# Kernel tuning notes

Measured on AMD Instinct MI355X. Metric: run time of the kernel, lower is better.

## Reference

```python
import jax, jax.numpy as jnp
import numpy as np

EPS = 1e-3  # Keras BatchNormalization default epsilon


def _bn(x, gamma, beta, mean, var):
    # inference-mode batchnorm over channel axis 1 of [N,C,T,V]
    s = (gamma * jax.lax.rsqrt(var + EPS)).reshape(1, -1, 1, 1)
    b = (beta - gamma * mean * jax.lax.rsqrt(var + EPS)).reshape(1, -1, 1, 1)
    return x * s + b


def setup_inputs() -> dict:
    key = jax.random.key(0)
    ks = jax.random.split(key, 10)
    N, C, T, V, K, F, KT = 64, 64, 300, 25, 3, 64, 9
    x = jax.random.normal(ks[0], (N, C, T, V), jnp.float32)
    W1 = jax.random.normal(ks[1], (C, F * K), jnp.float32) * 0.05
    b1 = jnp.zeros((F * K,), jnp.float32)
    A = jax.random.normal(ks[2], (K, T, V, V), jnp.float32) * 0.2
    gamma1 = jnp.ones((F,), jnp.float32)
    beta1 = jnp.zeros((F,), jnp.float32)
    mean1 = jax.random.normal(ks[3], (F,), jnp.float32) * 0.1
    var1 = jax.random.uniform(ks[4], (F,), jnp.float32) + 0.5
    Wt = jax.random.normal(ks[5], (KT, 1, F, F), jnp.float32) * 0.05  # HWIO
    bt = jnp.zeros((F,), jnp.float32)
    gamma2 = jnp.ones((F,), jnp.float32)
    beta2 = jnp.zeros((F,), jnp.float32)
    mean2 = jax.random.normal(ks[6], (F,), jnp.float32) * 0.1
    var2 = jax.random.uniform(ks[7], (F,), jnp.float32) + 0.5
    return dict(x=x, W1=W1, b1=b1, A=A, gamma1=gamma1, beta1=beta1,
                mean1=mean1, var1=var1, Wt=Wt, bt=bt, gamma2=gamma2,
                beta2=beta2, mean2=mean2, var2=var2)


def reference(x, W1, b1, A, gamma1, beta1, mean1, var1, Wt, bt,
              gamma2, beta2, mean2, var2):
    N, C, T, V = x.shape
    K = A.shape[0]
    F = W1.shape[1] // K
    # SGTACN: 1x1 conv (channels_first) == channel matmul
    y = jnp.einsum('nctv,cf->nftv', x, W1) + b1.reshape(1, -1, 1, 1)
    y = y.reshape(N, K, F, T, V)
    # spatial graph contraction with learned per-timestep adjacency
    y = jnp.einsum('nkftv,ktvw->nftw', y, A)
    # tgcn: BN -> relu -> temporal conv [9,1] SAME -> BN
    y = jax.nn.relu(_bn(y, gamma1, beta1, mean1, var1))
    y = jax.lax.conv_general_dilated(
        y, Wt, window_strides=(1, 1), padding='SAME',
        dimension_numbers=('NCHW', 'HWIO', 'NCHW')) + bt.reshape(1, -1, 1, 1)
    y = _bn(y, gamma2, beta2, mean2, var2)
    # identity residual (stride=1, no downsample, C_in == filters) + relu
    return jax.nn.relu(y + x)
```

## Files before the change

### kernel.cpp

```cpp
#include <hip/hip_runtime.h>
#include <hip/hip_bf16.h>
#include <stdint.h>

#define EPS 1e-3f

typedef __attribute__((ext_vector_type(8))) short bf16x8;
typedef __attribute__((ext_vector_type(4))) float f32x4;

__device__ inline uint32_t pk2(float a, float b) {
    __hip_bfloat162 p;
    p.x = __float2bfloat16(a);
    p.y = __float2bfloat16(b);
    return *(uint32_t*)&p;
}

__global__ __launch_bounds__(256) void k0_prep_small(
    const float* __restrict__ W1, const float* __restrict__ Wt,
    const float* __restrict__ A,
    uint16_t* __restrict__ W1t, uint16_t* __restrict__ Abf,
    float* __restrict__ csA_g)
{
    int i = blockIdx.x * 256 + threadIdx.x;
    if (i < 12288) {
        int f = i / 192, Kp = i % 192, k = Kp >> 6, c = Kp & 63;
        __hip_bfloat16 b = __float2bfloat16(W1[c * 192 + k * 64 + f]);
        W1t[i] = *(uint16_t*)&b;
    } else if (i < 49152) {
        int j = i - 12288;
        int jj = j & 7, fo = (j >> 3) & 63, kb = j >> 9;
        int kk = kb * 8 + jj, dt = kk >> 6, fi = kk & 63;
        __hip_bfloat16 b = __float2bfloat16(Wt[(dt * 64 + fi) * 64 + fo]);
        Abf[j] = *(uint16_t*)&b;
    } else if (i < 71652) {
        int j = i - 49152;
        int k = j / 7500, r = j % 7500;
        int t = r / 25, w = r % 25;
        float s = 0.f;
        for (int v = 0; v < 25; ++v)
            s += A[((k * 300 + t) * 25 + v) * 25 + w];
        csA_g[j] = s;
    }
}

__global__ __launch_bounds__(256) void k0_prep_At(
    const float* __restrict__ A, uint16_t* __restrict__ At_g)
{
    int i = blockIdx.x * 256 + threadIdx.x;
    if (i < 921600) {
        int v = i & 31, w = (i >> 5) & 31, rest = i >> 10;
        int t = rest % 300, k = rest / 300;
        float val = 0.f;
        if (v < 25 && w < 25)
            val = A[((k * 300 + t) * 25 + v) * 25 + w];
        __hip_bfloat16 b = __float2bfloat16(val);
        At_g[i] = *(uint16_t*)&b;
    }
}

#define K1_SMEM 39680
__global__ __launch_bounds__(256, 4) void k1_wave(
    const float* __restrict__ x, const uint16_t* __restrict__ At_g,
    const uint16_t* __restrict__ W1t, const float* __restrict__ csA_g,
    const float* __restrict__ b1,
    const float* __restrict__ gamma1, const float* __restrict__ beta1,
    const float* __restrict__ mean1, const float* __restrict__ var1,
    uint32_t* __restrict__ h2u)
{
    extern __shared__ __align__(16) char smem[];
    float* s1s   = (float*)(smem + 38400);
    float* b1ns  = (float*)(smem + 38656);
    float* b1s   = (float*)(smem + 38912);

    const int t0   = blockIdx.x * 4;
    const int n    = blockIdx.y;
    const int tid  = threadIdx.x;
    const int lane = tid & 63, wv = tid >> 6;
    const int l15  = lane & 15, g = lane >> 4;
    const int t    = t0 + wv;
    char* slab = smem + wv * 9600;

    bf16x8 bfr[6];
    #pragma unroll
    for (int nf = 0; nf < 6; ++nf) {
        const int col = nf * 16 + l15;
        const int k = col >> 5, w = col & 31;
        bfr[nf] = *(const bf16x8*)(At_g + (((k * 300 + t) * 32 + w) * 32 + g * 8));
    }

    const float* xb = x + (size_t)n * 480000 + t * 25;
    float xr8[4][8];
    float x24v[4];
    #pragma unroll
    for (int mf = 0; mf < 4; ++mf) {
        const int c = l15 + 16 * mf;
        const float* xr = xb + (size_t)c * 7500;
        if (g < 3) {
            const float* p = xr + g * 8;
            #pragma unroll
            for (int j = 0; j < 8; ++j) xr8[mf][j] = p[j];
        } else {
            x24v[mf] = xr[24];
        }
    }

    float cs[2][3];
    #pragma unroll
    for (int q = 0; q < 2; ++q) {
        const int w = q * 16 + l15;
        const int wc = (w < 25) ? w : 24;
        const int ci = t * 25 + wc;
        cs[q][0] = csA_g[ci];
        cs[q][1] = csA_g[7500 + ci];
        cs[q][2] = csA_g[15000 + ci];
    }

    __builtin_amdgcn_sched_barrier(0);

    if (tid < 64) {
        float rs = rsqrtf(var1[tid] + EPS);
        s1s[tid]  = gamma1[tid] * rs;
        b1ns[tid] = beta1[tid] - gamma1[tid] * mean1[tid] * rs;
    }
    if (tid >= 64 && tid < 256) b1s[tid - 64] = b1[tid - 64];
    __syncthreads();

    bf16x8 a[4];
    #pragma unroll
    for (int mf = 0; mf < 4; ++mf) {
        union { bf16x8 v; uint32_t u[4]; } ua;
        if (g < 3) {
            ua.u[0] = pk2(xr8[mf][0], xr8[mf][1]);
            ua.u[1] = pk2(xr8[mf][2], xr8[mf][3]);
            ua.u[2] = pk2(xr8[mf][4], xr8[mf][5]);
            ua.u[3] = pk2(xr8[mf][6], xr8[mf][7]);
        } else {
            ua.u[0] = pk2(x24v[mf], 0.f);
            ua.u[1] = 0; ua.u[2] = 0; ua.u[3] = 0;
        }
        a[mf] = ua.v;
    }

    #pragma unroll
    for (int hh = 0; hh < 2; ++hh) {
        f32x4 acc[4][3];
        #pragma unroll
        for (int mf = 0; mf < 4; ++mf)
            #pragma unroll
            for (int nf3 = 0; nf3 < 3; ++nf3)
                acc[mf][nf3] = (f32x4){0.f, 0.f, 0.f, 0.f};

        #pragma unroll
        for (int nf3 = 0; nf3 < 3; ++nf3) {
            const int nf = hh * 3 + nf3;
            acc[0][nf3] = __builtin_amdgcn_mfma_f32_16x16x32_bf16(a[0], bfr[nf], acc[0][nf3], 0, 0, 0);
            acc[1][nf3] = __builtin_amdgcn_mfma_f32_16x16x32_bf16(a[1], bfr[nf], acc[1][nf3], 0, 0, 0);
            acc[2][nf3] = __builtin_amdgcn_mfma_f32_16x16x32_bf16(a[2], bfr[nf], acc[2][nf3], 0, 0, 0);
            acc[3][nf3] = __builtin_amdgcn_mfma_f32_16x16x32_bf16(a[3], bfr[nf], acc[3][nf3], 0, 0, 0);
        }

        #pragma unroll
        for (int nf3 = 0; nf3 < 3; ++nf3) {
            const int col = (hh * 3 + nf3) * 16 + l15;
            const int k = col >> 5, w = col & 31;
            if (w < 25) {
                const int sw = (w & 7) << 4;
                #pragma unroll
                for (int mf = 0; mf < 4; ++mf) {
                    const int c0 = mf * 16 + g * 4;
                    const int off = w * 384 + (((k * 64 + c0) * 2) ^ sw);
                    uint2 val;
                    val.x = pk2(acc[mf][nf3][0], acc[mf][nf3][1]);
                    val.y = pk2(acc[mf][nf3][2], acc[mf][nf3][3]);
                    *(uint2*)(slab + off) = val;
                }
            }
        }
    }

    bf16x8 azc[4];
    #pragma unroll
    for (int mf = 0; mf < 4; ++mf)
        azc[mf] = *(const bf16x8*)(W1t + (l15 + 16 * mf) * 192 + g * 8);

    asm volatile("s_waitcnt lgkmcnt(0)" ::: "memory");
    __builtin_amdgcn_sched_barrier(0);

    int wq[2], qaddr[2], qswz[2];
    #pragma unroll
    for (int q = 0; q < 2; ++q) {
        int w = q * 16 + l15;
        wq[q] = w;
        int wc = (w < 25) ? w : 24;
        qaddr[q] = wc * 384;
        qswz[q]  = (wc & 7) << 4;
    }

    f32x4 accz[4][2];
    #pragma unroll
    for (int mf = 0; mf < 4; ++mf)
        #pragma unroll
        for (int q = 0; q < 2; ++q)
            accz[mf][q] = (f32x4){0.f, 0.f, 0.f, 0.f};

    #pragma unroll
    for (int kb = 0; kb < 6; ++kb) {
        bf16x8 azn[4];
        if (kb < 5) {
            #pragma unroll
            for (int mf = 0; mf < 4; ++mf)
                azn[mf] = *(const bf16x8*)(W1t + (l15 + 16 * mf) * 192 + (kb + 1) * 32 + g * 8);
        }
        #pragma unroll
        for (int q = 0; q < 2; ++q) {
            bf16x8 b = *(const bf16x8*)(slab + qaddr[q] + ((kb * 64 + g * 16) ^ qswz[q]));
            accz[0][q] = __builtin_amdgcn_mfma_f32_16x16x32_bf16(azc[0], b, accz[0][q], 0, 0, 0);
            accz[1][q] = __builtin_amdgcn_mfma_f32_16x16x32_bf16(azc[1], b, accz[1][q], 0, 0, 0);
            accz[2][q] = __builtin_amdgcn_mfma_f32_16x16x32_bf16(azc[2], b, accz[2][q], 0, 0, 0);
            accz[3][q] = __builtin_amdgcn_mfma_f32_16x16x32_bf16(azc[3], b, accz[3][q], 0, 0, 0);
        }
        if (kb < 5) {
            #pragma unroll
            for (int mf = 0; mf < 4; ++mf) azc[mf] = azn[mf];
        }
    }

    const uint32_t tb = (uint32_t)(n * 300 + t);
    #pragma unroll
    for (int q = 0; q < 2; ++q) {
        const int w = wq[q];
        if (w < 25) {
            const uint32_t rowbase = tb * 800 + w * 32;
            #pragma unroll
            for (int mf = 0; mf < 4; ++mf) {
                const int f0 = mf * 16 + g * 4;
                float zz[4];
                #pragma unroll
                for (int rg = 0; rg < 4; ++rg) {
                    const int f = f0 + rg;
                    float z = accz[mf][q][rg]
                            + b1s[f] * cs[q][0] + b1s[64 + f] * cs[q][1]
                            + b1s[128 + f] * cs[q][2];
                    z = z * s1s[f] + b1ns[f];
                    zz[rg] = fmaxf(z, 0.f);
                }
                uint2 st;
                st.x = pk2(zz[0], zz[1]);
                st.y = pk2(zz[2], zz[3]);
                *(uint2*)(h2u + rowbase + (f0 >> 1)) = st;
            }
        }
    }
}

#define K2_SMEM 51712
__global__ __launch_bounds__(256, 3) void k2_mfma(
    const char* __restrict__ h2b,
    const uint16_t* __restrict__ Abf,
    const float* __restrict__ bt,
    const float* __restrict__ gamma2, const float* __restrict__ beta2,
    const float* __restrict__ mean2,  const float* __restrict__ var2,
    const float* __restrict__ x,
    float* __restrict__ out)
{
    extern __shared__ __align__(16) char smem2[];
    char*  lds_h = smem2;
    float* s2s   = (float*)(smem2 + 51200);
    float* b2s   = s2s + 64;

    const int t0  = blockIdx.x * 8;
    const int n   = blockIdx.y;
    const int tid = threadIdx.x;

    const size_t hn = (size_t)n * 300 * 3200;
    int4 tmp[13];
    #pragma unroll
    for (int i = 0; i < 13; ++i) {
        const int c = tid + i * 256;
        tmp[i] = make_int4(0, 0, 0, 0);
        if (c < 3200) {
            int rr = c >> 3, c8 = c & 7;
            int trow = rr / 25;
            int w = rr - trow * 25;
            int tg = t0 - 4 + trow;
            if (tg >= 0 && tg < 300)
                tmp[i] = *(const int4*)(h2b + hn + (size_t)tg * 3200 + w * 128 + (c8 << 4));
        }
    }
    __builtin_amdgcn_sched_barrier(0);

    if (tid < 64) {
        float rs = rsqrtf(var2[tid] + EPS);
        float s  = gamma2[tid] * rs;
        s2s[tid] = s;
        b2s[tid] = beta2[tid] - gamma2[tid] * mean2[tid] * rs + bt[tid] * s;
    }

    #pragma unroll
    for (int i = 0; i < 13; ++i) {
        const int c = tid + i * 256;
        if (c < 3200) {
            int s = c << 4;
            *(int4*)(lds_h + (s ^ (((s >> 7) & 7) << 4))) = tmp[i];
        }
    }
    __syncthreads();

    const int wv = tid >> 6, lane = tid & 63;
    const int l15 = lane & 15, g = lane >> 4;
    const int nMf = (wv == 0) ? 4 : 3;

    int rbase[4];
    #pragma unroll
    for (int q = 0; q < 4; ++q) {
        int col = (q * 4 + wv) * 16 + l15;
        rbase[q] = (col < 200) ? col : 199;
    }

    f32x4 acc[4][4];
    #pragma unroll
    for (int q = 0; q < 4; ++q)
        #pragma unroll
        for (int mf = 0; mf < 4; ++mf)
            acc[q][mf] = (f32x4){0.f, 0.f, 0.f, 0.f};

    bf16x8 wc_[4];
    #pragma unroll
    for (int mf = 0; mf < 4; ++mf)
        wc_[mf] = *(const bf16x8*)(Abf + ((0 * 4 + g) * 64 + l15 + mf * 16) * 8);

    for (int kk = 0; kk < 18; ++kk) {
        const int dt   = kk >> 1;
        const int half = (kk & 1) << 6;
        bf16x8 wn_[4];
        if (kk < 17) {
            const int kbn = (kk + 1) * 4 + g;
            #pragma unroll
            for (int mf = 0; mf < 4; ++mf)
                wn_[mf] = *(const bf16x8*)(Abf + (kbn * 64 + l15 + mf * 16) * 8);
        }
        #pragma unroll
        for (int q = 0; q < 4; ++q) {
            if (q < nMf) {
                int r = rbase[q] + 25 * dt;
                int s = (r << 7) + half + (g << 4);
                bf16x8 hfr = *(const bf16x8*)(lds_h + (s ^ ((r & 7) << 4)));
                acc[q][0] = __builtin_amdgcn_mfma_f32_16x16x32_bf16(hfr, wc_[0], acc[q][0], 0, 0, 0);
                acc[q][1] = __builtin_amdgcn_mfma_f32_16x16x32_bf16(hfr, wc_[1], acc[q][1], 0, 0, 0);
                acc[q][2] = __builtin_amdgcn_mfma_f32_16x16x32_bf16(hfr, wc_[2], acc[q][2], 0, 0, 0);
                acc[q][3] = __builtin_amdgcn_mfma_f32_16x16x32_bf16(hfr, wc_[3], acc[q][3], 0, 0, 0);
            }
        }
        if (kk < 17) {
            #pragma unroll
            for (int mf = 0; mf < 4; ++mf) wc_[mf] = wn_[mf];
        }
    }

    const size_t outn = (size_t)n * 480000;
    const int base = t0 * 25;
    const int vcols = (7500 - base < 200) ? (7500 - base) : 200;

    float4 xrv[4][4];
    #pragma unroll
    for (int q = 0; q < 4; ++q) {
        const int col0 = (q * 4 + wv) * 16 + g * 4;
        if (q < nMf && col0 < vcols) {
            #pragma unroll
            for (int mf = 0; mf < 4; ++mf) {
                const int fo = mf * 16 + l15;
                xrv[q][mf] = *(const float4*)(x + outn + (size_t)fo * 7500 + base + col0);
            }
        }
    }
    __builtin_amdgcn_sched_barrier(0);

    #pragma unroll
    for (int q = 0; q < 4; ++q) {
        const int col0 = (q * 4 + wv) * 16 + g * 4;
        if (q < nMf && col0 < vcols) {
            #pragma unroll
            for (int mf = 0; mf < 4; ++mf) {
                const int fo = mf * 16 + l15;
                const size_t ga = outn + (size_t)fo * 7500 + base + col0;
                const float s2 = s2s[fo], b2 = b2s[fo];
                float4 o;
                o.x = fmaxf(acc[q][mf][0] * s2 + b2 + xrv[q][mf].x, 0.f);
                o.y = fmaxf(acc[q][mf][1] * s2 + b2 + xrv[q][mf].y, 0.f);
                o.z = fmaxf(acc[q][mf][2] * s2 + b2 + xrv[q][mf].z, 0.f);
                o.w = fmaxf(acc[q][mf][3] * s2 + b2 + xrv[q][mf].w, 0.f);
                *(float4*)(out + ga) = o;
            }
        }
    }
}

extern "C" void kernel_launch(void* const* d_in, const int* in_sizes, int n_in,
                              void* d_out, int out_size, void* d_ws, size_t ws_size,
                              hipStream_t stream) {
    const float* x      = (const float*)d_in[0];
    const float* W1     = (const float*)d_in[1];
    const float* b1     = (const float*)d_in[2];
    const float* A      = (const float*)d_in[3];
    const float* gamma1 = (const float*)d_in[4];
    const float* beta1  = (const float*)d_in[5];
    const float* mean1  = (const float*)d_in[6];
    const float* var1   = (const float*)d_in[7];
    const float* Wt     = (const float*)d_in[8];
    const float* bt     = (const float*)d_in[9];
    const float* gamma2 = (const float*)d_in[10];
    const float* beta2  = (const float*)d_in[11];
    const float* mean2  = (const float*)d_in[12];
    const float* var2   = (const float*)d_in[13];
    float* out = (float*)d_out;

    char* ws = (char*)d_ws;
    uint32_t* h2u   = (uint32_t*)ws;
    char*     h2b   = ws;
    uint16_t* At_g  = (uint16_t*)(ws + 61440000);
    uint16_t* W1t   = (uint16_t*)(ws + 63283200);
    uint16_t* Abf   = (uint16_t*)(ws + 63307776);
    float*    csA_g = (float*)   (ws + 63381504);

    hipFuncSetAttribute((const void*)k1_wave,
                        hipFuncAttributeMaxDynamicSharedMemorySize, K1_SMEM);
    hipFuncSetAttribute((const void*)k2_mfma,
                        hipFuncAttributeMaxDynamicSharedMemorySize, K2_SMEM);

    k0_prep_small<<<280, 256, 0, stream>>>(W1, Wt, A, W1t, Abf, csA_g);
    k0_prep_At<<<3600, 256, 0, stream>>>(A, At_g);
    k1_wave<<<dim3(75, 64), 256, K1_SMEM, stream>>>(
        x, At_g, W1t, csA_g, b1, gamma1, beta1, mean1, var1, h2u);
    k2_mfma<<<dim3(38, 64), 256, K2_SMEM, stream>>>(
        h2b, Abf, bt, gamma2, beta2, mean2, var2, x, out);
}
```

Measured before the change: 402.7 us.

## Process five timesteps per wave with prefetch, merge prep kernels

The first compute kernel now gives each wave five consecutive timesteps instead of one. The next timestep's adjacency and input values are loaded from global memory while the current timestep's second GEMM runs, and the block count drops accordingly. The two preprocessing kernels are merged into a single launch. The cost is fewer blocks (960), which lowers parallelism, plus more register pressure from the prefetch buffers.

Result: slower. 572.3 us (+42.1%).

```diff
diff --git a/kernel.cpp b/kernel.cpp
--- a/kernel.cpp
+++ b/kernel.cpp
@@ -14,46 +14,43 @@
     return *(uint32_t*)&p;
 }
 
-__global__ __launch_bounds__(256) void k0_prep_small(
+__global__ __launch_bounds__(256) void k0_prep(
     const float* __restrict__ W1, const float* __restrict__ Wt,
     const float* __restrict__ A,
     uint16_t* __restrict__ W1t, uint16_t* __restrict__ Abf,
-    float* __restrict__ csA_g)
+    float* __restrict__ csA_g, uint16_t* __restrict__ At_g)
 {
-    int i = blockIdx.x * 256 + threadIdx.x;
-    if (i < 12288) {
-        int f = i / 192, Kp = i % 192, k = Kp >> 6, c = Kp & 63;
-        __hip_bfloat16 b = __float2bfloat16(W1[c * 192 + k * 64 + f]);
-        W1t[i] = *(uint16_t*)&b;
-    } else if (i < 49152) {
-        int j = i - 12288;
-        int jj = j & 7, fo = (j >> 3) & 63, kb = j >> 9;
-        int kk = kb * 8 + jj, dt = kk >> 6, fi = kk & 63;
-        __hip_bfloat16 b = __float2bfloat16(Wt[(dt * 64 + fi) * 64 + fo]);
-        Abf[j] = *(uint16_t*)&b;
-    } else if (i < 71652) {
-        int j = i - 49152;
-        int k = j / 7500, r = j % 7500;
-        int t = r / 25, w = r % 25;
-        float s = 0.f;
-        for (int v = 0; v < 25; ++v)
-            s += A[((k * 300 + t) * 25 + v) * 25 + w];
-        csA_g[j] = s;
-    }
-}
-
-__global__ __launch_bounds__(256) void k0_prep_At(
-    const float* __restrict__ A, uint16_t* __restrict__ At_g)
-{
-    int i = blockIdx.x * 256 + threadIdx.x;
-    if (i < 921600) {
+    const int b = blockIdx.x;
+    if (b < 3600) {
+        int i = b * 256 + threadIdx.x;
         int v = i & 31, w = (i >> 5) & 31, rest = i >> 10;
         int t = rest % 300, k = rest / 300;
         float val = 0.f;
         if (v < 25 && w < 25)
             val = A[((k * 300 + t) * 25 + v) * 25 + w];
-        __hip_bfloat16 b = __float2bfloat16(val);
-        At_g[i] = *(uint16_t*)&b;
+        __hip_bfloat16 bb = __float2bfloat16(val);
+        At_g[i] = *(uint16_t*)&bb;
+    } else {
+        int i = (b - 3600) * 256 + threadIdx.x;
+        if (i < 12288) {
+            int f = i / 192, Kp = i % 192, k = Kp >> 6, c = Kp & 63;
+            __hip_bfloat16 bb = __float2bfloat16(W1[c * 192 + k * 64 + f]);
+            W1t[i] = *(uint16_t*)&bb;
+        } else if (i < 49152) {
+            int j = i - 12288;
+            int jj = j & 7, fo = (j >> 3) & 63, kb = j >> 9;
+            int kk = kb * 8 + jj, dt = kk >> 6, fi = kk & 63;
+            __hip_bfloat16 bb = __float2bfloat16(Wt[(dt * 64 + fi) * 64 + fo]);
+            Abf[j] = *(uint16_t*)&bb;
+        } else if (i < 71652) {
+            int j = i - 49152;
+            int k = j / 7500, r = j % 7500;
+            int t = r / 25, w = r % 25;
+            float s = 0.f;
+            for (int v = 0; v < 25; ++v)
+                s += A[((k * 300 + t) * 25 + v) * 25 + w];
+            csA_g[j] = s;
+        }
     }
 }
 
@@ -71,50 +68,13 @@
     float* b1ns  = (float*)(smem + 38656);
     float* b1s   = (float*)(smem + 38912);
 
-    const int t0   = blockIdx.x * 4;
+    const int t0   = blockIdx.x * 20;
     const int n    = blockIdx.y;
     const int tid  = threadIdx.x;
     const int lane = tid & 63, wv = tid >> 6;
     const int l15  = lane & 15, g = lane >> 4;
-    const int t    = t0 + wv;
+    const int tw0  = t0 + wv * 5;
     char* slab = smem + wv * 9600;
-
-    bf16x8 bfr[6];
-    #pragma unroll
-    for (int nf = 0; nf < 6; ++nf) {
-        const int col = nf * 16 + l15;
-        const int k = col >> 5, w = col & 31;
-        bfr[nf] = *(const bf16x8*)(At_g + (((k * 300 + t) * 32 + w) * 32 + g * 8));
-    }
-
-    const float* xb = x + (size_t)n * 480000 + t * 25;
-    float xr8[4][8];
-    float x24v[4];
-    #pragma unroll
-    for (int mf = 0; mf < 4; ++mf) {
-        const int c = l15 + 16 * mf;
-        const float* xr = xb + (size_t)c * 7500;
-        if (g < 3) {
-            const float* p = xr + g * 8;
-            #pragma unroll
-            for (int j = 0; j < 8; ++j) xr8[mf][j] = p[j];
-        } else {
-            x24v[mf] = xr[24];
-        }
-    }
-
-    float cs[2][3];
-    #pragma unroll
-    for (int q = 0; q < 2; ++q) {
-        const int w = q * 16 + l15;
-        const int wc = (w < 25) ? w : 24;
-        const int ci = t * 25 + wc;
-        cs[q][0] = csA_g[ci];
-        cs[q][1] = csA_g[7500 + ci];
-        cs[q][2] = csA_g[15000 + ci];
-    }
-
-    __builtin_amdgcn_sched_barrier(0);
 
     if (tid < 64) {
         float rs = rsqrtf(var1[tid] + EPS);
@@ -124,131 +84,159 @@
     if (tid >= 64 && tid < 256) b1s[tid - 64] = b1[tid - 64];
     __syncthreads();
 
-    bf16x8 a[4];
-    #pragma unroll
-    for (int mf = 0; mf < 4; ++mf) {
-        union { bf16x8 v; uint32_t u[4]; } ua;
-        if (g < 3) {
-            ua.u[0] = pk2(xr8[mf][0], xr8[mf][1]);
-            ua.u[1] = pk2(xr8[mf][2], xr8[mf][3]);
-            ua.u[2] = pk2(xr8[mf][4], xr8[mf][5]);
-            ua.u[3] = pk2(xr8[mf][6], xr8[mf][7]);
-        } else {
-            ua.u[0] = pk2(x24v[mf], 0.f);
-            ua.u[1] = 0; ua.u[2] = 0; ua.u[3] = 0;
-        }
-        a[mf] = ua.v;
-    }
-
-    #pragma unroll
-    for (int hh = 0; hh < 2; ++hh) {
-        f32x4 acc[4][3];
+    bf16x8 bfrN[6];
+    float  xr8[4][8];
+    float  x24v[4];
+    bf16x8 aN[4];
+
+    auto LOADT = [&](int t) {
+        #pragma unroll
+        for (int nf = 0; nf < 6; ++nf) {
+            const int col = nf * 16 + l15;
+            const int k = col >> 5, w = col & 31;
+            bfrN[nf] = *(const bf16x8*)(At_g + (((k * 300 + t) * 32 + w) * 32 + g * 8));
+        }
+        const float* xb = x + (size_t)n * 480000 + t * 25;
+        #pragma unroll
+        for (int mf = 0; mf < 4; ++mf) {
+            const int c = l15 + 16 * mf;
+            const float* xr = xb + (size_t)c * 7500;
+            if (g < 3) {
+                const float* p = xr + g * 8;
+                #pragma unroll
+                for (int j = 0; j < 8; ++j) xr8[mf][j] = p[j];
+            } else {
+                x24v[mf] = xr[24];
+            }
+        }
+    };
+    auto CONV = [&]() {
+        #pragma unroll
+        for (int mf = 0; mf < 4; ++mf) {
+            union { bf16x8 v; uint32_t u[4]; } ua;
+            if (g < 3) {
+                ua.u[0] = pk2(xr8[mf][0], xr8[mf][1]);
+                ua.u[1] = pk2(xr8[mf][2], xr8[mf][3]);
+                ua.u[2] = pk2(xr8[mf][4], xr8[mf][5]);
+                ua.u[3] = pk2(xr8[mf][6], xr8[mf][7]);
+            } else {
+                ua.u[0] = pk2(x24v[mf], 0.f);
+                ua.u[1] = 0; ua.u[2] = 0; ua.u[3] = 0;
+            }
+            aN[mf] = ua.v;
+        }
+    };
+
+    LOADT(tw0);
+    CONV();
+
+    #pragma unroll
+    for (int i = 0; i < 5; ++i) {
+        const int t = tw0 + i;
+
+        #pragma unroll
+        for (int hh = 0; hh < 2; ++hh) {
+            f32x4 acc[4][3];
+            #pragma unroll
+            for (int mf = 0; mf < 4; ++mf)
+                #pragma unroll
+                for (int nf3 = 0; nf3 < 3; ++nf3)
+                    acc[mf][nf3] = (f32x4){0.f, 0.f, 0.f, 0.f};
+
+            #pragma unroll
+            for (int nf3 = 0; nf3 < 3; ++nf3) {
+                const int nf = hh * 3 + nf3;
+                acc[0][nf3] = __builtin_amdgcn_mfma_f32_16x16x32_bf16(aN[0], bfrN[nf], acc[0][nf3], 0, 0, 0);
+                acc[1][nf3] = __builtin_amdgcn_mfma_f32_16x16x32_bf16(aN[1], bfrN[nf], acc[1][nf3], 0, 0, 0);
+                acc[2][nf3] = __builtin_amdgcn_mfma_f32_16x16x32_bf16(aN[2], bfrN[nf], acc[2][nf3], 0, 0, 0);
+                acc[3][nf3] = __builtin_amdgcn_mfma_f32_16x16x32_bf16(aN[3], bfrN[nf], acc[3][nf3], 0, 0, 0);
+            }
+
+            #pragma unroll
+            for (int nf3 = 0; nf3 < 3; ++nf3) {
+                const int col = (hh * 3 + nf3) * 16 + l15;
+                const int k = col >> 5, w = col & 31;
+                if (w < 25) {
+                    const int sw = (w & 7) << 4;
+                    #pragma unroll
+                    for (int mf = 0; mf < 4; ++mf) {
+                        const int c0 = mf * 16 + g * 4;
+                        const int off = w * 384 + (((k * 64 + c0) * 2) ^ sw);
+                        uint2 val;
+                        val.x = pk2(acc[mf][nf3][0], acc[mf][nf3][1]);
+                        val.y = pk2(acc[mf][nf3][2], acc[mf][nf3][3]);
+                        *(uint2*)(slab + off) = val;
+                    }
+                }
+            }
+        }
+
+        if (i < 4) LOADT(t + 1);
+
+        f32x4 accz[4][2];
         #pragma unroll
         for (int mf = 0; mf < 4; ++mf)
             #pragma unroll
-            for (int nf3 = 0; nf3 < 3; ++nf3)
-                acc[mf][nf3] = (f32x4){0.f, 0.f, 0.f, 0.f};
-
-        #pragma unroll
-        for (int nf3 = 0; nf3 < 3; ++nf3) {
-            const int nf = hh * 3 + nf3;
-            acc[0][nf3] = __builtin_amdgcn_mfma_f32_16x16x32_bf16(a[0], bfr[nf], acc[0][nf3], 0, 0, 0);
-            acc[1][nf3] = __builtin_amdgcn_mfma_f32_16x16x32_bf16(a[1], bfr[nf], acc[1][nf3], 0, 0, 0);
-            acc[2][nf3] = __builtin_amdgcn_mfma_f32_16x16x32_bf16(a[2], bfr[nf], acc[2][nf3], 0, 0, 0);
-            acc[3][nf3] = __builtin_amdgcn_mfma_f32_16x16x32_bf16(a[3], bfr[nf], acc[3][nf3], 0, 0, 0);
-        }
-
-        #pragma unroll
-        for (int nf3 = 0; nf3 < 3; ++nf3) {
-            const int col = (hh * 3 + nf3) * 16 + l15;
-            const int k = col >> 5, w = col & 31;
+            for (int q = 0; q < 2; ++q)
+                accz[mf][q] = (f32x4){0.f, 0.f, 0.f, 0.f};
+
+        int qaddr[2], qswz[2];
+        #pragma unroll
+        for (int q = 0; q < 2; ++q) {
+            int w = q * 16 + l15;
+            int wc = (w < 25) ? w : 24;
+            qaddr[q] = wc * 384;
+            qswz[q]  = (wc & 7) << 4;
+        }
+
+        #pragma unroll
+        for (int kb = 0; kb < 6; ++kb) {
+            bf16x8 az[4];
+            #pragma unroll
+            for (int mf = 0; mf < 4; ++mf)
+                az[mf] = *(const bf16x8*)(W1t + (l15 + 16 * mf) * 192 + kb * 32 + g * 8);
+            #pragma unroll
+            for (int q = 0; q < 2; ++q) {
+                bf16x8 b = *(const bf16x8*)(slab + qaddr[q] + ((kb * 64 + g * 16) ^ qswz[q]));
+                accz[0][q] = __builtin_amdgcn_mfma_f32_16x16x32_bf16(az[0], b, accz[0][q], 0, 0, 0);
+                accz[1][q] = __builtin_amdgcn_mfma_f32_16x16x32_bf16(az[1], b, accz[1][q], 0, 0, 0);
+                accz[2][q] = __builtin_amdgcn_mfma_f32_16x16x32_bf16(az[2], b, accz[2][q], 0, 0, 0);
+                accz[3][q] = __builtin_amdgcn_mfma_f32_16x16x32_bf16(az[3], b, accz[3][q], 0, 0, 0);
+            }
+        }
+
+        const uint32_t tb = (uint32_t)(n * 300 + t);
+        #pragma unroll
+        for (int q = 0; q < 2; ++q) {
+            const int w = q * 16 + l15;
             if (w < 25) {
-                const int sw = (w & 7) << 4;
+                const int ci = t * 25 + w;
+                const float cs0 = csA_g[ci];
+                const float cs1 = csA_g[7500 + ci];
+                const float cs2 = csA_g[15000 + ci];
+                const uint32_t rowbase = tb * 800 + w * 32;
                 #pragma unroll
                 for (int mf = 0; mf < 4; ++mf) {
-                    const int c0 = mf * 16 + g * 4;
-                    const int off = w * 384 + (((k * 64 + c0) * 2) ^ sw);
-                    uint2 val;
-                    val.x = pk2(acc[mf][nf3][0], acc[mf][nf3][1]);
-                    val.y = pk2(acc[mf][nf3][2], acc[mf][nf3][3]);
-                    *(uint2*)(slab + off) = val;
+                    const int f0 = mf * 16 + g * 4;
+                    float zz[4];
+                    #pragma unroll
+                    for (int rg = 0; rg < 4; ++rg) {
+                        const int f = f0 + rg;
+                        float z = accz[mf][q][rg]
+                                + b1s[f] * cs0 + b1s[64 + f] * cs1
+                                + b1s[128 + f] * cs2;
+                        z = z * s1s[f] + b1ns[f];
+                        zz[rg] = fmaxf(z, 0.f);
+                    }
+                    uint2 st;
+                    st.x = pk2(zz[0], zz[1]);
+                    st.y = pk2(zz[2], zz[3]);
+                    *(uint2*)(h2u + rowbase + (f0 >> 1)) = st;
                 }
             }
         }
-    }
-
-    bf16x8 azc[4];
-    #pragma unroll
-    for (int mf = 0; mf < 4; ++mf)
-        azc[mf] = *(const bf16x8*)(W1t + (l15 + 16 * mf) * 192 + g * 8);
-
-    asm volatile("s_waitcnt lgkmcnt(0)" ::: "memory");
-    __builtin_amdgcn_sched_barrier(0);
-
-    int wq[2], qaddr[2], qswz[2];
-    #pragma unroll
-    for (int q = 0; q < 2; ++q) {
-        int w = q * 16 + l15;
-        wq[q] = w;
-        int wc = (w < 25) ? w : 24;
-        qaddr[q] = wc * 384;
-        qswz[q]  = (wc & 7) << 4;
-    }
-
-    f32x4 accz[4][2];
-    #pragma unroll
-    for (int mf = 0; mf < 4; ++mf)
-        #pragma unroll
-        for (int q = 0; q < 2; ++q)
-            accz[mf][q] = (f32x4){0.f, 0.f, 0.f, 0.f};
-
-    #pragma unroll
-    for (int kb = 0; kb < 6; ++kb) {
-        bf16x8 azn[4];
-        if (kb < 5) {
-            #pragma unroll
-            for (int mf = 0; mf < 4; ++mf)
-                azn[mf] = *(const bf16x8*)(W1t + (l15 + 16 * mf) * 192 + (kb + 1) * 32 + g * 8);
-        }
-        #pragma unroll
-        for (int q = 0; q < 2; ++q) {
-            bf16x8 b = *(const bf16x8*)(slab + qaddr[q] + ((kb * 64 + g * 16) ^ qswz[q]));
-            accz[0][q] = __builtin_amdgcn_mfma_f32_16x16x32_bf16(azc[0], b, accz[0][q], 0, 0, 0);
-            accz[1][q] = __builtin_amdgcn_mfma_f32_16x16x32_bf16(azc[1], b, accz[1][q], 0, 0, 0);
-            accz[2][q] = __builtin_amdgcn_mfma_f32_16x16x32_bf16(azc[2], b, accz[2][q], 0, 0, 0);
-            accz[3][q] = __builtin_amdgcn_mfma_f32_16x16x32_bf16(azc[3], b, accz[3][q], 0, 0, 0);
-        }
-        if (kb < 5) {
-            #pragma unroll
-            for (int mf = 0; mf < 4; ++mf) azc[mf] = azn[mf];
-        }
-    }
-
-    const uint32_t tb = (uint32_t)(n * 300 + t);
-    #pragma unroll
-    for (int q = 0; q < 2; ++q) {
-        const int w = wq[q];
-        if (w < 25) {
-            const uint32_t rowbase = tb * 800 + w * 32;
-            #pragma unroll
-            for (int mf = 0; mf < 4; ++mf) {
-                const int f0 = mf * 16 + g * 4;
-                float zz[4];
-                #pragma unroll
-                for (int rg = 0; rg < 4; ++rg) {
-                    const int f = f0 + rg;
-                    float z = accz[mf][q][rg]
-                            + b1s[f] * cs[q][0] + b1s[64 + f] * cs[q][1]
-                            + b1s[128 + f] * cs[q][2];
-                    z = z * s1s[f] + b1ns[f];
-                    zz[rg] = fmaxf(z, 0.f);
-                }
-                uint2 st;
-                st.x = pk2(zz[0], zz[1]);
-                st.y = pk2(zz[2], zz[3]);
-                *(uint2*)(h2u + rowbase + (f0 >> 1)) = st;
-            }
-        }
+
+        if (i < 4) CONV();
     }
 }
 
@@ -426,9 +414,8 @@
     hipFuncSetAttribute((const void*)k2_mfma,
                         hipFuncAttributeMaxDynamicSharedMemorySize, K2_SMEM);
 
-    k0_prep_small<<<280, 256, 0, stream>>>(W1, Wt, A, W1t, Abf, csA_g);
-    k0_prep_At<<<3600, 256, 0, stream>>>(A, At_g);
-    k1_wave<<<dim3(75, 64), 256, K1_SMEM, stream>>>(
+    k0_prep<<<3880, 256, 0, stream>>>(W1, Wt, A, W1t, Abf, csA_g, At_g);
+    k1_wave<<<dim3(15, 64), 256, K1_SMEM, stream>>>(
         x, At_g, W1t, csA_g, b1, gamma1, beta1, mean1, var1, h2u);
     k2_mfma<<<dim3(38, 64), 256, K2_SMEM, stream>>>(
         h2b, Abf, bt, gamma2, beta2, mean2, var2, x, out);
```
